# Kernel optimization log

Hardware: AMD Instinct MI355X
Metric: run time of the kernel (lower is better)

Reference implementation:

```python
import jax, jax.numpy as jnp
import numpy as np

D_MODEL = 1024
N_HEADS = 16
D_HEAD = D_MODEL // N_HEADS
B, L = 4, 2048
NEG_INF = float('-inf')


def setup_inputs() -> dict:
    key = jax.random.key(0)
    ks = jax.random.split(key, 8)
    x = jax.random.normal(ks[0], (B, L, D_MODEL), dtype=jnp.float32)
    # sorted cumulative event times in hours (~0-2000h span)
    timestamps = jnp.cumsum(jax.random.uniform(ks[1], (B, L), dtype=jnp.float32), axis=-1)
    mask = jnp.ones((B, L), dtype=jnp.float32)
    s = 1.0 / np.sqrt(D_MODEL)
    W_qkv = jax.random.normal(ks[2], (3 * D_MODEL, D_MODEL), dtype=jnp.float32) * s
    b_qkv = jnp.zeros((3 * D_MODEL,), dtype=jnp.float32)
    W_out = jax.random.normal(ks[3], (D_MODEL, D_MODEL), dtype=jnp.float32) * s
    b_out = jnp.zeros((D_MODEL,), dtype=jnp.float32)
    decay_rate = jnp.full((N_HEADS,), 0.01, dtype=jnp.float32)
    return {"x": x, "timestamps": timestamps, "mask": mask,
            "W_qkv": W_qkv, "b_qkv": b_qkv, "W_out": W_out, "b_out": b_out,
            "decay_rate": decay_rate}


def reference(x, timestamps, mask, W_qkv, b_qkv, W_out, b_out, decay_rate):
    Bb, Ll, Dd = x.shape
    H, dh = N_HEADS, D_HEAD
    scale = dh ** (-0.5)
    qkv = x @ W_qkv.T + b_qkv                     # (B,L,3D)
    qkv = qkv.reshape(Bb, Ll, 3, H, dh).transpose(2, 0, 3, 1, 4)  # (3,B,H,L,dh)
    q, k, v = qkv[0], qkv[1], qkv[2]
    attn = jnp.einsum('bhqd,bhkd->bhqk', q, k) * scale
    t_diff = jnp.abs(timestamps[:, :, None] - timestamps[:, None, :])[:, None]  # (B,1,L,L)
    decay = jax.nn.softplus(decay_rate)[None, :, None, None]                    # (1,H,1,1)
    attn = attn - decay * t_diff / 24.0
    causal = jnp.triu(jnp.ones((Ll, Ll), dtype=bool), k=1)        # (L,L) True above diag
    attn = jnp.where(causal[None, None], NEG_INF, attn)
    pad = (mask == 0.0)[:, None, None, :]                         # (B,1,1,L) True=pad key
    attn = jnp.where(pad, NEG_INF, attn)
    attn = jax.nn.softmax(attn, axis=-1)
    out = jnp.einsum('bhqk,bhkd->bhqd', attn, v)                  # (B,H,L,dh)
    out = out.transpose(0, 2, 1, 3).reshape(Bb, Ll, Dd)
    return out @ W_out.T + b_out
```

## Files before the change

### kernel.cpp

```cpp
#include <hip/hip_runtime.h>
#include <stdint.h>
#include <math.h>

#define B_   4
#define L_   2048
#define H_   16
#define DH_  64
#define DM_  1024

typedef __bf16 bf16;
typedef __attribute__((ext_vector_type(8))) __bf16 bf16x8;
typedef __attribute__((ext_vector_type(4))) float f32x4;
typedef __attribute__((ext_vector_type(4))) int i32x4;
typedef __attribute__((ext_vector_type(4))) short s16x4;
typedef unsigned short u16;
typedef unsigned int u32;
typedef __attribute__((ext_vector_type(2))) unsigned int u32x2;
typedef __attribute__((ext_vector_type(4))) unsigned short u16x4;

typedef unsigned int u32g __attribute__((address_space(1)));
typedef unsigned int u32l __attribute__((address_space(3)));

__device__ __forceinline__ u16 f2bf(float f) {
  return __builtin_bit_cast(u16, (bf16)f);
}

__device__ __forceinline__ float exp2_fast(float x) {
  float r; asm("v_exp_f32 %0, %1" : "=v"(r) : "v"(x)); return r;
}

__device__ __forceinline__ void gload16(const void* g, void* l) {
  __builtin_amdgcn_global_load_lds((const u32g*)g, (u32l*)l, 16, 0, 0);
}

__device__ __forceinline__ f32x4 mfma16(s16x4 a, s16x4 b, f32x4 c) {
#if __has_builtin(__builtin_amdgcn_mfma_f32_16x16x16bf16_1k)
  return __builtin_amdgcn_mfma_f32_16x16x16bf16_1k(a, b, c, 0, 0, 0);
#else
  asm volatile("v_mfma_f32_16x16x16_bf16 %0, %1, %2, %0\n\ts_nop 7\n\ts_nop 2"
               : "+v"(c) : "v"(a), "v"(b));
  return c;
#endif
}

__global__ __launch_bounds__(256) void cvt_f32_bf16(const float* __restrict__ src,
                                                    u16* __restrict__ dst, int n4) {
  int i = blockIdx.x * 256 + threadIdx.x;
  if (i >= n4) return;
  f32x4 v = ((const f32x4*)src)[i];
  u16x4 o;
  o[0] = f2bf(v[0]); o[1] = f2bf(v[1]); o[2] = f2bf(v[2]); o[3] = f2bf(v[3]);
  ((u16x4*)dst)[i] = o;
}

__global__ __launch_bounds__(256) void bias_fill(const float* __restrict__ ts,
                                                 const float* __restrict__ msk,
                                                 const float* __restrict__ decay,
                                                 float* __restrict__ Bk) {
  int i = blockIdx.x * 256 + threadIdx.x;
  int bh = i >> 11, l = i & (L_ - 1);
  int b = bh >> 4, h = bh & 15;
  float dc24 = log1pf(__expf(decay[h])) * (1.0f / 24.0f) * 1.44269504f;
  float tv = ts[b * L_ + l], mv = msk[b * L_ + l];
  Bk[i] = (mv != 0.f) ? dc24 * tv : -INFINITY;
}

__global__ __launch_bounds__(512) void gemm_bf16(
    const u16* __restrict__ A, const u16* __restrict__ Bm, const float* __restrict__ bias,
    int M, int N, int K, int mode,
    u16* __restrict__ Qb, u16* __restrict__ Kb, u16* __restrict__ Vt, float* __restrict__ Cout)
{
  __shared__ char smem[147456];
  u16* ltr = (u16*)smem;

  const int tid = threadIdx.x;
  const int nwg = gridDim.x;
  int idx = blockIdx.x;
  idx = (idx & 7) * (nwg >> 3) + (idx >> 3);
  const int nbx = N >> 7;
  const int bx = idx % nbx, by = idx / nbx;
  const int m0 = by << 8, n0 = bx << 7;

  const int lane = tid & 63, w = tid >> 6;
  const int g = lane >> 4, col = lane & 15;
  const int wr = w >> 1, wc = w & 1;

  f32x4 acc[4][4];
#pragma unroll
  for (int mt = 0; mt < 4; ++mt)
#pragma unroll
    for (int nt = 0; nt < 4; ++nt) {
      acc[mt][nt][0] = 0.f; acc[mt][nt][1] = 0.f;
      acc[mt][nt][2] = 0.f; acc[mt][nt][3] = 0.f;
    }

  auto STAGEG = [&](int kt, int nb) {
    char* dA = smem + nb * 49152;
    char* dB = dA + 32768;
    const int k0 = kt << 6;
#pragma unroll
    for (int pp = 0; pp < 4; ++pp) {
      int c = tid + pp * 512;
      int row = c >> 3, cc = c & 7;
      gload16(A + (size_t)(m0 + row) * K + k0 + ((cc ^ (row & 7)) << 3), dA + c * 16);
    }
#pragma unroll
    for (int pp = 0; pp < 2; ++pp) {
      int c = tid + pp * 512;
      int row = c >> 3, cc = c & 7;
      gload16(Bm + (size_t)(n0 + row) * K + k0 + ((cc ^ (row & 7)) << 3), dB + c * 16);
    }
  };

  STAGEG(0, 0);
  STAGEG(1, 1);
  asm volatile("s_waitcnt vmcnt(6)" ::: "memory");
  __builtin_amdgcn_s_barrier();

  const int nk = K >> 6;
  for (int t = 0; t < nk; ++t) {
    const char* bufA = smem + (t % 3) * 49152;
    const char* bufB = bufA + 32768;
#pragma unroll
    for (int kk = 0; kk < 2; ++kk) {
      bf16x8 af[4], bfr[4];
#pragma unroll
      for (int mt = 0; mt < 4; ++mt) {
        int row = wr * 64 + mt * 16 + col;
        af[mt] = *(const bf16x8*)(bufA + row * 128 + ((((kk << 2) + g) ^ (row & 7)) << 4));
      }
#pragma unroll
      for (int nt = 0; nt < 4; ++nt) {
        int row = wc * 64 + nt * 16 + col;
        bfr[nt] = *(const bf16x8*)(bufB + row * 128 + ((((kk << 2) + g) ^ (row & 7)) << 4));
      }
      if (kk == 0 && t + 2 < nk) STAGEG(t + 2, (t + 2) % 3);
      __builtin_amdgcn_s_barrier();
      asm volatile("s_waitcnt lgkmcnt(0)" ::: "memory");
      __builtin_amdgcn_sched_barrier(0);
      __builtin_amdgcn_s_setprio(1);
#pragma unroll
      for (int mt = 0; mt < 4; ++mt)
#pragma unroll
        for (int nt = 0; nt < 4; ++nt)
          acc[mt][nt] = __builtin_amdgcn_mfma_f32_16x16x32_bf16(af[mt], bfr[nt], acc[mt][nt], 0, 0, 0);
      __builtin_amdgcn_s_setprio(0);
      if (kk == 1) {
        if (t + 2 < nk)      asm volatile("s_waitcnt vmcnt(6)" ::: "memory");
        else if (t + 1 < nk) asm volatile("s_waitcnt vmcnt(0)" ::: "memory");
      }
      __builtin_amdgcn_s_barrier();
    }
  }

  if (mode == 1) {
#pragma unroll
    for (int nt = 0; nt < 4; ++nt) {
      int gn = n0 + wc * 64 + nt * 16 + col;
      float bv = bias[gn];
#pragma unroll
      for (int mt = 0; mt < 4; ++mt) {
        int mbase = m0 + wr * 64 + mt * 16 + g * 4;
#pragma unroll
        for (int r = 0; r < 4; ++r)
          Cout[(size_t)(mbase + r) * N + gn] = acc[mt][nt][r] + bv;
      }
    }
    return;
  }

  const int type = n0 >> 10;
  const float qsc = (type == 0) ? 0.125f * 1.44269504f : 1.0f;
#pragma unroll
  for (int nt = 0; nt < 4; ++nt) {
    int nn = wc * 64 + nt * 16 + col;
    float bv = bias[n0 + nn];
#pragma unroll
    for (int mt = 0; mt < 4; ++mt) {
      int mm = wr * 64 + mt * 16 + g * 4;
#pragma unroll
      for (int r = 0; r < 4; ++r) {
        u16 hv = f2bf((acc[mt][nt][r] + bv) * qsc);
        if (type < 2) ltr[(mm + r) * 136 + nn] = hv;
        else          ltr[nn * 264 + (mm + r)] = hv;
      }
    }
  }
  __syncthreads();
  if (type < 2) {
#pragma unroll
    for (int it = 0; it < 8; ++it) {
      int cid = tid + it * 512;
      int rrow = cid >> 4, cc = cid & 15;
      i32x4 v = *(const i32x4*)((const char*)ltr + rrow * 272 + cc * 16);
      int token = m0 + rrow;
      int bb = token >> 11, ll = token & (L_ - 1);
      int gn = n0 + cc * 8;
      int head = (gn & 1023) >> 6, d = gn & 63;
      u16* dst = (type == 0) ? Qb : Kb;
      *(i32x4*)(dst + ((size_t)((bb * H_ + head) * L_ + ll)) * 64 + d) = v;
    }
  } else {
#pragma unroll
    for (int it = 0; it < 8; ++it) {
      int cid = tid + it * 512;
      int rrow = cid >> 5, cc = cid & 31;
      i32x4 v = *(const i32x4*)((const char*)ltr + rrow * 528 + cc * 16);
      int gn = n0 + rrow;
      int head = (gn & 1023) >> 6, d = gn & 63;
      int token0 = m0 + cc * 8;
      int bb = token0 >> 11, ll = token0 & (L_ - 1);
      *(i32x4*)(Vt + ((size_t)((bb * H_ + head) * DH_ + d)) * L_ + ll) = v;
    }
  }
}

__global__ __launch_bounds__(512, 2) void attn_fwd(
    const u16* __restrict__ Qb, const u16* __restrict__ Kb, const u16* __restrict__ Vt,
    const float* __restrict__ Bk, u16* __restrict__ AO)
{
  __shared__ u16 lK[3][64 * 64];
  __shared__ u16 lV[3][64 * 64];

  const int phys = blockIdx.x;
  const int xcd = phys & 7, s = phys >> 3;
  const int bh = xcd * 8 + (s >> 3);
  const int pr = s & 7;
  const int qa = pr, qbt = 15 - pr;
  const int b = bh >> 4, h = bh & 15;

  const int tid = threadIdx.x, w = tid >> 6, lane = tid & 63;
  const int g = lane >> 4, q16 = lane & 15;

  const float* Bkb = Bk + (size_t)bh * L_;

  int kcol[2], vcol[4];
#pragma unroll
  for (int kk = 0; kk < 2; ++kk) kcol[kk] = ((kk * 4 + g) ^ (q16 & 7)) << 4;
#pragma unroll
  for (int t = 0; t < 4; ++t)
    vcol[t] = (((2 * t + (g >> 1)) ^ (q16 & 7)) << 4) + (g & 1) * 8;

  const int nkA = (qa + 1) * 2;
  const int nkB = (qbt + 1) * 2;

  auto STAGE = [&](int gst, int nb) {
    const int kt = (gst < nkA) ? gst : gst - nkA;
    const int kg0 = kt * 64;
    const int r8 = tid >> 3, cc = tid & 7;
    gload16(Kb + ((size_t)bh * L_ + kg0 + r8) * 64 + ((cc ^ (r8 & 7)) * 8),
            (char*)lK[nb] + tid * 16);
    gload16(Vt + ((size_t)(bh * 64 + r8)) * L_ + kg0 + ((cc ^ (r8 & 7)) * 8),
            (char*)lV[nb] + tid * 16);
  };

  auto BODY = [&](bf16x8 (&qf)[2], f32x4 (&o)[4], float& m_r, float& l_r,
                  int qrow, int kg0, int cur) {
    f32x4 sv[4];
#pragma unroll
    for (int t = 0; t < 4; ++t)
      sv[t] = *(const f32x4*)(Bkb + kg0 + t * 16 + g * 4);

    __builtin_amdgcn_s_setprio(1);
#pragma unroll
    for (int t = 0; t < 4; ++t) {
      const char* krow = (const char*)lK[cur] + t * 2048 + q16 * 128;
#pragma unroll
      for (int kk = 0; kk < 2; ++kk) {
        bf16x8 kf = *(const bf16x8*)(krow + kcol[kk]);
        sv[t] = __builtin_amdgcn_mfma_f32_16x16x32_bf16(kf, qf[kk], sv[t], 0, 0, 0);
      }
    }
    __builtin_amdgcn_s_setprio(0);

    if (kg0 + 63 > qrow) {
      const int qg = qrow + q16;
#pragma unroll
      for (int t = 0; t < 4; ++t)
#pragma unroll
        for (int r = 0; r < 4; ++r)
          sv[t][r] = (kg0 + t * 16 + g * 4 + r <= qg) ? sv[t][r] : -INFINITY;
    }

    float mx = fmaxf(sv[0][0], sv[0][1]);
    mx = fmaxf(mx, fmaxf(sv[0][2], sv[0][3]));
#pragma unroll
    for (int t = 1; t < 4; ++t) {
      mx = fmaxf(mx, fmaxf(sv[t][0], sv[t][1]));
      mx = fmaxf(mx, fmaxf(sv[t][2], sv[t][3]));
    }
    mx = fmaxf(mx, __shfl_xor(mx, 16));
    mx = fmaxf(mx, __shfl_xor(mx, 32));

    float mn = m_r;
    if (__any(mx > m_r + 8.f)) {
      mn = fmaxf(m_r, mx);
      float al = exp2_fast(m_r - mn);
      m_r = mn;
      l_r *= al;
#pragma unroll
      for (int db = 0; db < 4; ++db) {
        o[db][0] *= al; o[db][1] *= al; o[db][2] *= al; o[db][3] *= al;
      }
    }
    float rs = 0.f;
#pragma unroll
    for (int t = 0; t < 4; ++t)
#pragma unroll
      for (int r = 0; r < 4; ++r) {
        float pv = exp2_fast(sv[t][r] - mn);
        sv[t][r] = pv;
        rs += pv;
      }
    l_r += rs;

    s16x4 pf[4];
#pragma unroll
    for (int t = 0; t < 4; ++t) {
      s16x4 pp;
      pp[0] = (short)f2bf(sv[t][0]); pp[1] = (short)f2bf(sv[t][1]);
      pp[2] = (short)f2bf(sv[t][2]); pp[3] = (short)f2bf(sv[t][3]);
      pf[t] = pp;
    }

    __builtin_amdgcn_s_setprio(1);
#pragma unroll
    for (int t = 0; t < 4; ++t) {
      const char* vrow = (const char*)lV[cur] + q16 * 128 + vcol[t];
#pragma unroll
      for (int db = 0; db < 4; ++db) {
        s16x4 vf = *(const s16x4*)(vrow + db * 2048);
        o[db] = mfma16(vf, pf[t], o[db]);
      }
    }
    __builtin_amdgcn_s_setprio(0);
  };

  auto EPI = [&](f32x4 (&o)[4], float l_r, int qt) {
    float lt = l_r + __shfl_xor(l_r, 16);
    lt += __shfl_xor(lt, 32);
    float inv = 1.f / lt;
    u16* dst = AO + ((size_t)(b * L_ + qt * 128 + w * 16 + q16)) * DM_ + h * 64 + g * 4;
#pragma unroll
    for (int db = 0; db < 4; ++db) {
      u32x2 pk;
      pk[0] = (u32)f2bf(o[db][0] * inv) | ((u32)f2bf(o[db][1] * inv) << 16);
      pk[1] = (u32)f2bf(o[db][2] * inv) | ((u32)f2bf(o[db][3] * inv) << 16);
      *(u32x2*)(dst + db * 16) = pk;
    }
  };

  STAGE(0, 0);
  STAGE(1, 1);
  asm volatile("s_waitcnt vmcnt(2) lgkmcnt(0)" ::: "memory");
  __builtin_amdgcn_s_barrier();
  __builtin_amdgcn_sched_barrier(0);

  {
    const int qrow = qa * 128 + w * 16;
    const int mkt = (qrow + 79) >> 6;
    bf16x8 qf[2];
    {
      const u16* Qr = Qb + ((size_t)bh * L_ + qrow + q16) * 64;
      qf[0] = *(const bf16x8*)(Qr + g * 8);
      qf[1] = *(const bf16x8*)(Qr + 32 + g * 8);
    }
    float m_r = -INFINITY, l_r = 0.f;
    f32x4 o[4];
#pragma unroll
    for (int db = 0; db < 4; ++db) {
      o[db][0] = 0.f; o[db][1] = 0.f; o[db][2] = 0.f; o[db][3] = 0.f;
    }
    for (int st = 0; st < nkA; ++st) {
      const int cur = st % 3;
      STAGE(st + 2, (st + 2) % 3);
      if (st < mkt) BODY(qf, o, m_r, l_r, qrow, st * 64, cur);
      asm volatile("s_waitcnt vmcnt(2) lgkmcnt(0)" ::: "memory");
      __builtin_amdgcn_s_barrier();
      __builtin_amdgcn_sched_barrier(0);
    }
    EPI(o, l_r, qa);
  }

  {
    const int qrow = qbt * 128 + w * 16;
    const int mkt = (qrow + 79) >> 6;
    bf16x8 qf[2];
    {
      const u16* Qr = Qb + ((size_t)bh * L_ + qrow + q16) * 64;
      qf[0] = *(const bf16x8*)(Qr + g * 8);
      qf[1] = *(const bf16x8*)(Qr + 32 + g * 8);
    }
    float m_r = -INFINITY, l_r = 0.f;
    f32x4 o[4];
#pragma unroll
    for (int db = 0; db < 4; ++db) {
      o[db][0] = 0.f; o[db][1] = 0.f; o[db][2] = 0.f; o[db][3] = 0.f;
    }
    for (int kt = 0; kt < nkB; ++kt) {
      const int gst = nkA + kt;
      const int cur = gst % 3;
      const bool pf = (kt + 2 < nkB);
      if (pf) STAGE(gst + 2, (gst + 2) % 3);
      if (kt < mkt) BODY(qf, o, m_r, l_r, qrow, kt * 64, cur);
      if (kt + 1 < nkB) {
        if (pf) asm volatile("s_waitcnt vmcnt(2) lgkmcnt(0)" ::: "memory");
        else    asm volatile("s_waitcnt vmcnt(0) lgkmcnt(0)" ::: "memory");
        __builtin_amdgcn_s_barrier();
        __builtin_amdgcn_sched_barrier(0);
      }
    }
    EPI(o, l_r, qbt);
  }
}

extern "C" void kernel_launch(void* const* d_in, const int* in_sizes, int n_in,
                              void* d_out, int out_size, void* d_ws, size_t ws_size,
                              hipStream_t stream) {
  const float* x    = (const float*)d_in[0];
  const float* ts   = (const float*)d_in[1];
  const float* mk   = (const float*)d_in[2];
  const float* Wqkv = (const float*)d_in[3];
  const float* bqkv = (const float*)d_in[4];
  const float* Wout = (const float*)d_in[5];
  const float* bout = (const float*)d_in[6];
  const float* dec  = (const float*)d_in[7];
  float* out = (float*)d_out;

  char* ws = (char*)d_ws;
  u16* xbf  = (u16*)(ws + 0);
  u16* wqbf = (u16*)(ws + 16777216);
  u16* wobf = (u16*)(ws + 23068672);
  u16* Qb   = (u16*)(ws + 25165824);
  u16* Kb   = (u16*)(ws + 41943040);
  u16* Vt   = (u16*)(ws + 58720256);
  u16* AO   = (u16*)(ws + 75497472);
  float* Bk = (float*)(ws + 92274688);

  cvt_f32_bf16<<<dim3(8192 * 1024 / 4 / 256), 256, 0, stream>>>(x, xbf, 8192 * 1024 / 4);
  cvt_f32_bf16<<<dim3(3072 * 1024 / 4 / 256), 256, 0, stream>>>(Wqkv, wqbf, 3072 * 1024 / 4);
  cvt_f32_bf16<<<dim3(1024 * 1024 / 4 / 256), 256, 0, stream>>>(Wout, wobf, 1024 * 1024 / 4);

  bias_fill<<<dim3(64 * 2048 / 256), 256, 0, stream>>>(ts, mk, dec, Bk);

  gemm_bf16<<<dim3(768), 512, 0, stream>>>(
      xbf, wqbf, bqkv, 8192, 3072, 1024, 0, Qb, Kb, Vt, nullptr);

  attn_fwd<<<dim3(512), 512, 0, stream>>>(Qb, Kb, Vt, Bk, AO);

  gemm_bf16<<<dim3(256), 512, 0, stream>>>(
      AO, wobf, bout, 8192, 1024, 1024, 1, nullptr, nullptr, nullptr, out);
}
```

Before: 192.8 us.

## Merge GEMM k-substep barriers and prefetch attention key-bias one tile ahead

In the GEMM loop, the per-substep barrier pairs become a single wait-and-barrier per K tile, with the LDS waits folded into it. In the attention kernel, the per-key bias vector load is issued one tile ahead into registers, so the global load latency overlaps the previous tile's compute. The vmcnt thresholds are raised to cover the extra outstanding bias loads. Dropping the barrier between the two k-substeps relies on the triple buffer staying ahead of the refill, and the prefetch costs extra registers.

```diff
diff --git a/kernel.cpp b/kernel.cpp
--- a/kernel.cpp
+++ b/kernel.cpp
@@ -135,9 +135,6 @@
         bfr[nt] = *(const bf16x8*)(bufB + row * 128 + ((((kk << 2) + g) ^ (row & 7)) << 4));
       }
       if (kk == 0 && t + 2 < nk) STAGEG(t + 2, (t + 2) % 3);
-      __builtin_amdgcn_s_barrier();
-      asm volatile("s_waitcnt lgkmcnt(0)" ::: "memory");
-      __builtin_amdgcn_sched_barrier(0);
       __builtin_amdgcn_s_setprio(1);
 #pragma unroll
       for (int mt = 0; mt < 4; ++mt)
@@ -145,12 +142,11 @@
         for (int nt = 0; nt < 4; ++nt)
           acc[mt][nt] = __builtin_amdgcn_mfma_f32_16x16x32_bf16(af[mt], bfr[nt], acc[mt][nt], 0, 0, 0);
       __builtin_amdgcn_s_setprio(0);
-      if (kk == 1) {
-        if (t + 2 < nk)      asm volatile("s_waitcnt vmcnt(6)" ::: "memory");
-        else if (t + 1 < nk) asm volatile("s_waitcnt vmcnt(0)" ::: "memory");
-      }
-      __builtin_amdgcn_s_barrier();
-    }
+    }
+    if (t + 2 < nk)      asm volatile("s_waitcnt vmcnt(6) lgkmcnt(0)" ::: "memory");
+    else if (t + 1 < nk) asm volatile("s_waitcnt vmcnt(0) lgkmcnt(0)" ::: "memory");
+    else                 asm volatile("s_waitcnt lgkmcnt(0)" ::: "memory");
+    __builtin_amdgcn_s_barrier();
   }
 
   if (mode == 1) {
@@ -243,6 +239,7 @@
 
   const int nkA = (qa + 1) * 2;
   const int nkB = (qbt + 1) * 2;
+  const int ns  = nkA + nkB;
 
   auto STAGE = [&](int gst, int nb) {
     const int kt = (gst < nkA) ? gst : gst - nkA;
@@ -254,13 +251,17 @@
             (char*)lV[nb] + tid * 16);
   };
 
+  f32x4 bkp[4];
+  auto BIASPF = [&](int gst) {
+    const int kt = (gst < nkA) ? gst : gst - nkA;
+    const int kg0 = kt * 64;
+#pragma unroll
+    for (int t = 0; t < 4; ++t)
+      bkp[t] = *(const f32x4*)(Bkb + kg0 + t * 16 + g * 4);
+  };
+
   auto BODY = [&](bf16x8 (&qf)[2], f32x4 (&o)[4], float& m_r, float& l_r,
-                  int qrow, int kg0, int cur) {
-    f32x4 sv[4];
-#pragma unroll
-    for (int t = 0; t < 4; ++t)
-      sv[t] = *(const f32x4*)(Bkb + kg0 + t * 16 + g * 4);
-
+                  int qrow, int kg0, int cur, f32x4 (&sv)[4]) {
     __builtin_amdgcn_s_setprio(1);
 #pragma unroll
     for (int t = 0; t < 4; ++t) {
@@ -350,6 +351,7 @@
     }
   };
 
+  BIASPF(0);
   STAGE(0, 0);
   STAGE(1, 1);
   asm volatile("s_waitcnt vmcnt(2) lgkmcnt(0)" ::: "memory");
@@ -374,8 +376,12 @@
     for (int st = 0; st < nkA; ++st) {
       const int cur = st % 3;
       STAGE(st + 2, (st + 2) % 3);
-      if (st < mkt) BODY(qf, o, m_r, l_r, qrow, st * 64, cur);
-      asm volatile("s_waitcnt vmcnt(2) lgkmcnt(0)" ::: "memory");
+      f32x4 sv[4];
+#pragma unroll
+      for (int t = 0; t < 4; ++t) sv[t] = bkp[t];
+      BIASPF(st + 1);
+      if (st < mkt) BODY(qf, o, m_r, l_r, qrow, st * 64, cur, sv);
+      asm volatile("s_waitcnt vmcnt(6) lgkmcnt(0)" ::: "memory");
       __builtin_amdgcn_s_barrier();
       __builtin_amdgcn_sched_barrier(0);
     }
@@ -402,10 +408,14 @@
       const int cur = gst % 3;
       const bool pf = (kt + 2 < nkB);
       if (pf) STAGE(gst + 2, (gst + 2) % 3);
-      if (kt < mkt) BODY(qf, o, m_r, l_r, qrow, kt * 64, cur);
+      f32x4 sv[4];
+#pragma unroll
+      for (int t = 0; t < 4; ++t) sv[t] = bkp[t];
+      BIASPF(gst + 1 < ns ? gst + 1 : 0);
+      if (kt < mkt) BODY(qf, o, m_r, l_r, qrow, kt * 64, cur, sv);
       if (kt + 1 < nkB) {
-        if (pf) asm volatile("s_waitcnt vmcnt(2) lgkmcnt(0)" ::: "memory");
-        else    asm volatile("s_waitcnt vmcnt(0) lgkmcnt(0)" ::: "memory");
+        if (pf) asm volatile("s_waitcnt vmcnt(6) lgkmcnt(0)" ::: "memory");
+        else    asm volatile("s_waitcnt vmcnt(4) lgkmcnt(0)" ::: "memory");
         __builtin_amdgcn_s_barrier();
         __builtin_amdgcn_sched_barrier(0);
       }
```

Result: slower. 197.2 us (+2.3%).

## Interleave GEMM LDS reads, prefetch, and MFMA in quadrants; merge conversion kernels

Applied to the files above, without the earlier changes.

The GEMM main loop now splits each k-tile's work into four 2x2 MFMA quadrants that cover both k-halves. LDS fragment reads and the next-stage global-to-LDS prefetch are spread across those phases so memory traffic overlaps tensor-core work. The three fp32-to-bf16 conversion launches are merged into one kernel that picks its source by index range, removing two launches. The cost is more barriers per k-tile and extra register pressure from holding both k-halves of the fragments.

```diff
diff --git a/kernel.cpp b/kernel.cpp
--- a/kernel.cpp
+++ b/kernel.cpp
@@ -43,14 +43,23 @@
 #endif
 }
 
-__global__ __launch_bounds__(256) void cvt_f32_bf16(const float* __restrict__ src,
-                                                    u16* __restrict__ dst, int n4) {
+#define NX4 2097152
+#define NQ4 786432
+#define NO4 262144
+__global__ __launch_bounds__(256) void cvt3(const float* __restrict__ x,
+                                            const float* __restrict__ wq,
+                                            const float* __restrict__ wo,
+                                            u16* __restrict__ xb, u16* __restrict__ wqb,
+                                            u16* __restrict__ wob) {
   int i = blockIdx.x * 256 + threadIdx.x;
-  if (i >= n4) return;
-  f32x4 v = ((const f32x4*)src)[i];
+  const float* src; u16* dst; int j;
+  if (i < NX4)            { src = x;  dst = xb;  j = i; }
+  else if (i < NX4 + NQ4) { src = wq; dst = wqb; j = i - NX4; }
+  else                    { src = wo; dst = wob; j = i - NX4 - NQ4; }
+  f32x4 v = ((const f32x4*)src)[j];
   u16x4 o;
   o[0] = f2bf(v[0]); o[1] = f2bf(v[1]); o[2] = f2bf(v[2]); o[3] = f2bf(v[3]);
-  ((u16x4*)dst)[i] = o;
+  ((u16x4*)dst)[j] = o;
 }
 
 __global__ __launch_bounds__(256) void bias_fill(const float* __restrict__ ts,
@@ -94,16 +103,19 @@
       acc[mt][nt][2] = 0.f; acc[mt][nt][3] = 0.f;
     }
 
-  auto STAGEG = [&](int kt, int nb) {
+  auto STAGE_A = [&](int kt, int nb, int hh) {
     char* dA = smem + nb * 49152;
-    char* dB = dA + 32768;
     const int k0 = kt << 6;
 #pragma unroll
-    for (int pp = 0; pp < 4; ++pp) {
+    for (int pp = hh * 2; pp < hh * 2 + 2; ++pp) {
       int c = tid + pp * 512;
       int row = c >> 3, cc = c & 7;
       gload16(A + (size_t)(m0 + row) * K + k0 + ((cc ^ (row & 7)) << 3), dA + c * 16);
     }
+  };
+  auto STAGE_B = [&](int kt, int nb) {
+    char* dB = smem + nb * 49152 + 32768;
+    const int k0 = kt << 6;
 #pragma unroll
     for (int pp = 0; pp < 2; ++pp) {
       int c = tid + pp * 512;
@@ -112,8 +124,8 @@
     }
   };
 
-  STAGEG(0, 0);
-  STAGEG(1, 1);
+  STAGE_A(0, 0, 0); STAGE_A(0, 0, 1); STAGE_B(0, 0);
+  STAGE_A(1, 1, 0); STAGE_A(1, 1, 1); STAGE_B(1, 1);
   asm volatile("s_waitcnt vmcnt(6)" ::: "memory");
   __builtin_amdgcn_s_barrier();
 
@@ -121,36 +133,64 @@
   for (int t = 0; t < nk; ++t) {
     const char* bufA = smem + (t % 3) * 49152;
     const char* bufB = bufA + 32768;
-#pragma unroll
-    for (int kk = 0; kk < 2; ++kk) {
-      bf16x8 af[4], bfr[4];
-#pragma unroll
-      for (int mt = 0; mt < 4; ++mt) {
-        int row = wr * 64 + mt * 16 + col;
-        af[mt] = *(const bf16x8*)(bufA + row * 128 + ((((kk << 2) + g) ^ (row & 7)) << 4));
-      }
-#pragma unroll
-      for (int nt = 0; nt < 4; ++nt) {
-        int row = wc * 64 + nt * 16 + col;
-        bfr[nt] = *(const bf16x8*)(bufB + row * 128 + ((((kk << 2) + g) ^ (row & 7)) << 4));
-      }
-      if (kk == 0 && t + 2 < nk) STAGEG(t + 2, (t + 2) % 3);
-      __builtin_amdgcn_s_barrier();
-      asm volatile("s_waitcnt lgkmcnt(0)" ::: "memory");
-      __builtin_amdgcn_sched_barrier(0);
+    const bool pf = (t + 2 < nk);
+    const int nb2 = (t + 2) % 3;
+
+    bf16x8 af[4][2], bfr[4][2];
+    auto RDA = [&](int mt, int kk) {
+      int row = wr * 64 + mt * 16 + col;
+      return *(const bf16x8*)(bufA + row * 128 + ((((kk << 2) + g) ^ (row & 7)) << 4));
+    };
+    auto RDB = [&](int nt, int kk) {
+      int row = wc * 64 + nt * 16 + col;
+      return *(const bf16x8*)(bufB + row * 128 + ((((kk << 2) + g) ^ (row & 7)) << 4));
+    };
+    auto QUAD = [&](int qm, int qn) {
       __builtin_amdgcn_s_setprio(1);
 #pragma unroll
-      for (int mt = 0; mt < 4; ++mt)
-#pragma unroll
-        for (int nt = 0; nt < 4; ++nt)
-          acc[mt][nt] = __builtin_amdgcn_mfma_f32_16x16x32_bf16(af[mt], bfr[nt], acc[mt][nt], 0, 0, 0);
+      for (int mi = 0; mi < 2; ++mi)
+#pragma unroll
+        for (int ni = 0; ni < 2; ++ni)
+#pragma unroll
+          for (int kk = 0; kk < 2; ++kk)
+            acc[qm * 2 + mi][qn * 2 + ni] = __builtin_amdgcn_mfma_f32_16x16x32_bf16(
+                af[qm * 2 + mi][kk], bfr[qn * 2 + ni][kk], acc[qm * 2 + mi][qn * 2 + ni], 0, 0, 0);
       __builtin_amdgcn_s_setprio(0);
-      if (kk == 1) {
-        if (t + 2 < nk)      asm volatile("s_waitcnt vmcnt(6)" ::: "memory");
-        else if (t + 1 < nk) asm volatile("s_waitcnt vmcnt(0)" ::: "memory");
-      }
-      __builtin_amdgcn_s_barrier();
-    }
+    };
+
+#pragma unroll
+    for (int mi = 0; mi < 2; ++mi) { af[mi][0] = RDA(mi, 0); af[mi][1] = RDA(mi, 1); }
+#pragma unroll
+    for (int ni = 0; ni < 2; ++ni) { bfr[ni][0] = RDB(ni, 0); bfr[ni][1] = RDB(ni, 1); }
+    if (pf) STAGE_A(t + 2, nb2, 0);
+    __builtin_amdgcn_s_barrier();
+    asm volatile("s_waitcnt lgkmcnt(0)" ::: "memory");
+    __builtin_amdgcn_sched_barrier(0);
+    QUAD(0, 0);
+    __builtin_amdgcn_s_barrier();
+
+#pragma unroll
+    for (int ni = 2; ni < 4; ++ni) { bfr[ni][0] = RDB(ni, 0); bfr[ni][1] = RDB(ni, 1); }
+    if (pf) STAGE_A(t + 2, nb2, 1);
+    __builtin_amdgcn_s_barrier();
+    asm volatile("s_waitcnt lgkmcnt(0)" ::: "memory");
+    __builtin_amdgcn_sched_barrier(0);
+    QUAD(0, 1);
+    __builtin_amdgcn_s_barrier();
+
+#pragma unroll
+    for (int mi = 2; mi < 4; ++mi) { af[mi][0] = RDA(mi, 0); af[mi][1] = RDA(mi, 1); }
+    if (pf) STAGE_B(t + 2, nb2);
+    __builtin_amdgcn_s_barrier();
+    asm volatile("s_waitcnt lgkmcnt(0)" ::: "memory");
+    __builtin_amdgcn_sched_barrier(0);
+    QUAD(1, 1);
+    __builtin_amdgcn_s_barrier();
+
+    QUAD(1, 0);
+    if (pf)              asm volatile("s_waitcnt vmcnt(6)" ::: "memory");
+    else if (t + 1 < nk) asm volatile("s_waitcnt vmcnt(0)" ::: "memory");
+    __builtin_amdgcn_s_barrier();
   }
 
   if (mode == 1) {
@@ -437,9 +477,7 @@
   u16* AO   = (u16*)(ws + 75497472);
   float* Bk = (float*)(ws + 92274688);
 
-  cvt_f32_bf16<<<dim3(8192 * 1024 / 4 / 256), 256, 0, stream>>>(x, xbf, 8192 * 1024 / 4);
-  cvt_f32_bf16<<<dim3(3072 * 1024 / 4 / 256), 256, 0, stream>>>(Wqkv, wqbf, 3072 * 1024 / 4);
-  cvt_f32_bf16<<<dim3(1024 * 1024 / 4 / 256), 256, 0, stream>>>(Wout, wobf, 1024 * 1024 / 4);
+  cvt3<<<dim3((NX4 + NQ4 + NO4) / 256), 256, 0, stream>>>(x, Wqkv, Wout, xbf, wqbf, wobf);
 
   bias_fill<<<dim3(64 * 2048 / 256), 256, 0, stream>>>(ts, mk, dec, Bk);
 
```

New measurement: 191.2 us. No clear change (-0.8%).
